# Kernel optimization log

Hardware: AMD Instinct MI355X
Metric: run time of the kernel (lower is better)

The kernel has to match this reference:

```python
import jax, jax.numpy as jnp
import numpy as np

B, T, D, H = 4, 1024, 1024, 16
HD = D // H
DFF = 2048          # ExpertTier hidden width
K = 3               # ConvTier causal kernel size
NEG = -1e9


def layernorm(x, w, b, eps=1e-5):
    m = jnp.mean(x, axis=-1, keepdims=True)
    v = jnp.var(x, axis=-1, keepdims=True)
    return (x - m) * jax.lax.rsqrt(v + eps) * w + b


def rope_cos_sin(t, hd):
    inv = 1.0 / (10000.0 ** (jnp.arange(0, hd, 2, dtype=jnp.float32) / hd))
    freqs = jnp.outer(jnp.arange(t, dtype=jnp.float32), inv)  # (T, hd/2)
    return jnp.cos(freqs), jnp.sin(freqs)


def apply_rope(x, cos, sin):
    # x: (B, H, T, hd); cos/sin: (T, hd/2)
    x1, x2 = jnp.split(x, 2, axis=-1)
    return jnp.concatenate([x1 * cos - x2 * sin, x1 * sin + x2 * cos], axis=-1)


def causal_attn(q, k, v):
    # q,k,v: (..., T, d); full causal softmax attention
    t = q.shape[-2]
    scale = 1.0 / jnp.sqrt(jnp.asarray(q.shape[-1], q.dtype))
    scores = jnp.einsum('...qd,...kd->...qk', q, k) * scale
    mask = jnp.triu(jnp.ones((t, t), dtype=bool), k=1)
    scores = jnp.where(mask, NEG, scores)
    w = jax.nn.softmax(scores, axis=-1)
    return jnp.einsum('...qk,...kd->...qd', w, v)


def setup_inputs() -> dict:
    key = jax.random.key(0)
    ks = jax.random.split(key, 16)
    ws = 0.02
    g = lambda k, shape, s: jax.random.normal(k, shape, dtype=jnp.float32) * s
    return {
        'x': g(ks[0], (B, T, D), 1.0),
        'ln1_w': jnp.ones((D,), jnp.float32), 'ln1_b': jnp.zeros((D,), jnp.float32),
        'qkv_w': g(ks[1], (D, 3 * D), ws),
        'out_w': g(ks[2], (D, D), ws),
        'ln2_w': jnp.ones((D,), jnp.float32), 'ln2_b': jnp.zeros((D,), jnp.float32),
        'router_w': g(ks[3], (D, 4), ws),
        'conv_w': g(ks[4], (D, 1, K), 0.1),             # depthwise OIW, groups=D
        'expert_w1': g(ks[5], (D, DFF), ws),
        'expert_w2': g(ks[6], (DFF, D), ws),
        'at_wq': g(ks[7], (D, D), ws),
        'at_wk': g(ks[8], (D, D), ws),
        'at_wv': g(ks[9], (D, D), ws),
        'at_wo': g(ks[10], (D, D), ws),
        'tier_gate': jnp.full((D,), 0.1, jnp.float32),
        'sink_kv_scale': jnp.asarray(0.1, jnp.float32),
    }


def reference(x, ln1_w, ln1_b, qkv_w, out_w, ln2_w, ln2_b, router_w, conv_w,
              expert_w1, expert_w2, at_wq, at_wk, at_wv, at_wo,
              tier_gate, sink_kv_scale):
    b, t, d = x.shape
    # --- backbone causal self-attention with RoPE (pre-norm) ---
    h1 = layernorm(x, ln1_w, ln1_b)
    qkv = (h1 @ qkv_w).reshape(b, t, 3, H, HD)
    q = qkv[:, :, 0].transpose(0, 2, 1, 3)  # (B,H,T,hd)
    k = qkv[:, :, 1].transpose(0, 2, 1, 3)
    v = qkv[:, :, 2].transpose(0, 2, 1, 3)
    cos, sin = rope_cos_sin(t, HD)
    q = apply_rope(q, cos, sin)
    k = apply_rope(k, cos, sin)
    ao = causal_attn(q, k, v)                         # (B,H,T,hd)
    ao = ao.transpose(0, 2, 1, 3).reshape(b, t, d) @ out_w
    x = x + ao
    # --- router + tiers ---
    h = layernorm(x, ln2_w, ln2_b)
    routing_w = jax.nn.softmax(h @ router_w, axis=-1)  # (B,T,4): conv/expert/attn/sink
    # ConvTier: depthwise causal conv (k=3) + GELU
    hc = jnp.pad(h.transpose(0, 2, 1), ((0, 0), (0, 0), (K - 1, 0)))  # (B,D,T+K-1)
    conv = jax.lax.conv_general_dilated(hc, conv_w, (1,), 'VALID',
                                        feature_group_count=d,
                                        dimension_numbers=('NCH', 'OIH', 'NCH'))
    conv_out = jax.nn.gelu(conv.transpose(0, 2, 1))   # (B,T,D)
    # ExpertTier: 2-layer GELU MLP
    expert_out = jax.nn.gelu(h @ expert_w1) @ expert_w2
    # AttentionTier: single-head causal attention
    attn2 = causal_attn(h @ at_wq, h @ at_wk, h @ at_wv) @ at_wo
    # SinkTier outputs zeros -> contributes nothing to the weighted sum
    combined = (conv_out * routing_w[..., 0:1]
                + expert_out * routing_w[..., 1:2]
                + attn2 * routing_w[..., 2:3])
    x = x + combined * tier_gate
    # sink kv scaling
    kv_scale = 1.0 - routing_w[..., 3] * (1.0 - jnp.abs(sink_kv_scale))
    x = x * kv_scale[..., None]
    return (x, routing_w)
```

## Files before the change

### kernel.cpp

```cpp
#include <hip/hip_runtime.h>

#define Bz 4
#define Tz 1024
#define Dz 1024
#define Hz 16
#define NTz (Bz*Tz)

typedef short s8v __attribute__((ext_vector_type(8)));
typedef float f4v __attribute__((ext_vector_type(4)));

__device__ __forceinline__ float bf2f(unsigned short u){
  unsigned int x = ((unsigned int)u) << 16;
  return __builtin_bit_cast(float, x);
}
__device__ __forceinline__ unsigned short f2bf(float f){
  unsigned int x = __builtin_bit_cast(unsigned int, f);
  x += 0x7fffu + ((x >> 16) & 1u);
  return (unsigned short)(x >> 16);
}
__device__ __forceinline__ float gelu_f(float x){
  float z = 1.5957691216057308f * (x + 0.044715f * x * x * x);
  return x / (1.0f + __expf(-z));
}
__device__ __forceinline__ void gl16(const unsigned short* g, unsigned short* l){
  __builtin_amdgcn_global_load_lds(
      (const __attribute__((address_space(1))) unsigned int*)g,
      (__attribute__((address_space(3))) unsigned int*)l, 16, 0, 0);
}

struct WSeg { const float* in; unsigned short* out; int R, C, blk0, bx; };
struct WPack { WSeg s[8]; };
__global__ __launch_bounds__(256) void k_convtrans_all(WPack p)
{
  __shared__ float tile[32][33];
  int bid = blockIdx.x;
  const float* in = p.s[0].in; unsigned short* out = p.s[0].out;
  int R = p.s[0].R, C = p.s[0].C, blk0 = 0, bx = p.s[0].bx;
  #pragma unroll
  for (int i = 1; i < 8; ++i) {
    if (bid >= p.s[i].blk0) {
      in = p.s[i].in; out = p.s[i].out; R = p.s[i].R; C = p.s[i].C;
      blk0 = p.s[i].blk0; bx = p.s[i].bx;
    }
  }
  int rel = bid - blk0;
  int c0 = (rel % bx) * 32, r0 = (rel / bx) * 32;
  int tx = threadIdx.x & 31, ty = threadIdx.x >> 5;
  #pragma unroll
  for (int i = 0; i < 32; i += 8)
    tile[ty + i][tx] = in[(long)(r0 + ty + i) * C + c0 + tx];
  __syncthreads();
  #pragma unroll
  for (int i = 0; i < 32; i += 8)
    out[(long)(c0 + ty + i) * R + r0 + tx] = f2bf(tile[tx][ty + i]);
}

__global__ __launch_bounds__(256) void k_convtrans_b(const unsigned short* __restrict__ in,
    unsigned short* __restrict__ out, int ld, long sIn, long sOut)
{
  __shared__ unsigned short tile[32][34];
  in  += (long)blockIdx.z * sIn;
  out += (long)blockIdx.z * sOut;
  int c0 = blockIdx.x * 32, r0 = blockIdx.y * 32;
  int tx = threadIdx.x & 31, ty = threadIdx.x >> 5;
  #pragma unroll
  for (int i = 0; i < 32; i += 8)
    tile[ty + i][tx] = in[(long)(r0 + ty + i) * ld + c0 + tx];
  __syncthreads();
  #pragma unroll
  for (int i = 0; i < 32; i += 8)
    out[(long)(c0 + ty + i) * 1024 + r0 + tx] = tile[tx][ty + i];
}

__global__ __launch_bounds__(256) void k_layernorm(const float* __restrict__ x,
    const float* __restrict__ w, const float* __restrict__ b,
    unsigned short* __restrict__ out)
{
  int row = blockIdx.x, tid = threadIdx.x;
  const float4* xp = (const float4*)(x + (long)row * Dz);
  float4 v = xp[tid];
  float s  = v.x + v.y + v.z + v.w;
  float ss = v.x*v.x + v.y*v.y + v.z*v.z + v.w*v.w;
  int lane = tid & 63, wv = tid >> 6;
  #pragma unroll
  for (int off = 32; off; off >>= 1){ s += __shfl_xor(s, off); ss += __shfl_xor(ss, off); }
  __shared__ float red[8];
  if (lane == 0){ red[wv] = s; red[4 + wv] = ss; }
  __syncthreads();
  s  = red[0] + red[1] + red[2] + red[3];
  ss = red[4] + red[5] + red[6] + red[7];
  float mean = s * (1.0f / Dz);
  float var  = ss * (1.0f / Dz) - mean * mean;
  float rstd = rsqrtf(var + 1e-5f);
  float4 wg = ((const float4*)w)[tid];
  float4 bg = ((const float4*)b)[tid];
  ushort4 ov;
  ov.x = f2bf((v.x - mean) * rstd * wg.x + bg.x);
  ov.y = f2bf((v.y - mean) * rstd * wg.y + bg.y);
  ov.z = f2bf((v.z - mean) * rstd * wg.z + bg.z);
  ov.w = f2bf((v.w - mean) * rstd * wg.w + bg.w);
  *((ushort4*)(out + (long)row * Dz) + tid) = ov;
}

__global__ __launch_bounds__(256) void k_ln_router(const float* __restrict__ x,
    const float* __restrict__ w, const float* __restrict__ b,
    const float* __restrict__ rw, unsigned short* __restrict__ out,
    float* __restrict__ rout)
{
  int row = blockIdx.x, tid = threadIdx.x;
  const float4* xp = (const float4*)(x + (long)row * Dz);
  float4 v = xp[tid];
  float s  = v.x + v.y + v.z + v.w;
  float ss = v.x*v.x + v.y*v.y + v.z*v.z + v.w*v.w;
  int lane = tid & 63, wv = tid >> 6;
  #pragma unroll
  for (int off = 32; off; off >>= 1){ s += __shfl_xor(s, off); ss += __shfl_xor(ss, off); }
  __shared__ float red[8];
  if (lane == 0){ red[wv] = s; red[4 + wv] = ss; }
  __syncthreads();
  s  = red[0] + red[1] + red[2] + red[3];
  ss = red[4] + red[5] + red[6] + red[7];
  float mean = s * (1.0f / Dz);
  float var  = ss * (1.0f / Dz) - mean * mean;
  float rstd = rsqrtf(var + 1e-5f);
  float4 wg = ((const float4*)w)[tid];
  float4 bg = ((const float4*)b)[tid];
  float h0 = (v.x - mean) * rstd * wg.x + bg.x;
  float h1 = (v.y - mean) * rstd * wg.y + bg.y;
  float h2 = (v.z - mean) * rstd * wg.z + bg.z;
  float h3 = (v.w - mean) * rstd * wg.w + bg.w;
  ushort4 ov;
  ov.x = f2bf(h0); ov.y = f2bf(h1); ov.z = f2bf(h2); ov.w = f2bf(h3);
  *((ushort4*)(out + (long)row * Dz) + tid) = ov;
  int d0 = tid * 4;
  float4 r0 = *(const float4*)(rw + (long)d0 * 4);
  float4 r1 = *(const float4*)(rw + (long)(d0 + 1) * 4);
  float4 r2 = *(const float4*)(rw + (long)(d0 + 2) * 4);
  float4 r3 = *(const float4*)(rw + (long)(d0 + 3) * 4);
  float a0 = h0*r0.x + h1*r1.x + h2*r2.x + h3*r3.x;
  float a1 = h0*r0.y + h1*r1.y + h2*r2.y + h3*r3.y;
  float a2 = h0*r0.z + h1*r1.z + h2*r2.z + h3*r3.z;
  float a3 = h0*r0.w + h1*r1.w + h2*r2.w + h3*r3.w;
  #pragma unroll
  for (int off = 32; off; off >>= 1) {
    a0 += __shfl_xor(a0, off); a1 += __shfl_xor(a1, off);
    a2 += __shfl_xor(a2, off); a3 += __shfl_xor(a3, off);
  }
  __shared__ float red2[4][4];
  if (lane == 0){ red2[wv][0] = a0; red2[wv][1] = a1; red2[wv][2] = a2; red2[wv][3] = a3; }
  __syncthreads();
  if (tid == 0) {
    float s0 = red2[0][0] + red2[1][0] + red2[2][0] + red2[3][0];
    float s1 = red2[0][1] + red2[1][1] + red2[2][1] + red2[3][1];
    float s2 = red2[0][2] + red2[1][2] + red2[2][2] + red2[3][2];
    float s3 = red2[0][3] + red2[1][3] + red2[2][3] + red2[3][3];
    float mx = fmaxf(fmaxf(s0, s1), fmaxf(s2, s3));
    float e0 = __expf(s0 - mx), e1 = __expf(s1 - mx);
    float e2 = __expf(s2 - mx), e3 = __expf(s3 - mx);
    float inv = 1.0f / (e0 + e1 + e2 + e3);
    float4 r = {e0 * inv, e1 * inv, e2 * inv, e3 * inv};
    *(float4*)(rout + (long)row * 4) = r;
  }
}

template<int MODE, int BN, bool TRIMAP, bool TRIK, bool DBUF>
__global__ __launch_bounds__(256) void k_gemm(
    const unsigned short* __restrict__ A,
    const unsigned short* __restrict__ Bt,
    float* __restrict__ Cf, unsigned short* __restrict__ Cb,
    const float* __restrict__ addsrc,
    unsigned short* __restrict__ P1, unsigned short* __restrict__ P2,
    int N, int K, int lda, int ldb,
    long sA, long sB, long sC)
{
  constexpr int BM = 128;
  constexpr int MREP = (BN == 128) ? 4 : 2;
  constexpr int NB = DBUF ? 2 : 1;
  __shared__ unsigned short As[NB][BM * 64];
  __shared__ unsigned short Bs[NB][BN * 64];
  int bm, bn;
  if (TRIMAP) {
    int li = blockIdx.x;
    int nwg = gridDim.x;
    if ((nwg & 7) == 0) li = (li & 7) * (nwg >> 3) + (li >> 3);
    int r = (int)((sqrtf(4.f * li + 1.f) - 1.f) * 0.5f);
    if ((r + 1) * (r + 2) <= li) ++r;
    if (r * (r + 1) > li) --r;
    bm = r * 128; bn = (li - r * (r + 1)) * BN;
  } else {
    int lin = blockIdx.y * gridDim.x + blockIdx.x;
    int nwg = gridDim.x * gridDim.y;
    if ((nwg & 7) == 0) lin = (lin & 7) * (nwg >> 3) + (lin >> 3);
    int cols = gridDim.x, rows = gridDim.y;
    constexpr int GM = 8;
    int in_grp = GM * cols;
    int gid = lin / in_grp;
    int fm = gid * GM;
    int gsz = min(rows - fm, GM);
    int rem = lin - gid * in_grp;
    int pm = fm + (rem % gsz);
    int pn = rem / gsz;
    if (TRIK) pm = rows - 1 - pm;
    bm = pm * BM; bn = pn * BN;
  }
  A  += (long)blockIdx.z * sA;
  Bt += (long)blockIdx.z * sB;
  int tid = threadIdx.x, w = tid >> 6, lane = tid & 63;
  int wr, wc;
  if (BN == 128) { wr = (w >> 1) * 64; wc = (w & 1) * 64; }
  else           { wr = w * 32;        wc = 0; }
  f4v acc[MREP][4];
  #pragma unroll
  for (int m = 0; m < MREP; ++m)
    #pragma unroll
    for (int n = 0; n < 4; ++n)
      acc[m][n] = (f4v){0.f, 0.f, 0.f, 0.f};

  int Keff = K;
  if (TRIK) Keff = min(K, bm + BM);

  int lrow = lane >> 3;
  int lcol = (((lane & 7) ^ lrow) * 8);
  const unsigned short* AgJ[4];
  int AsOff[4];
  #pragma unroll
  for (int j = 0; j < 4; ++j) {
    AgJ[j] = A + (long)(bm + w * 32 + j * 8 + lrow) * lda + lcol;
    AsOff[j] = (w * 32 + j * 8) * 64;
  }
  constexpr int BCH = BN / 8 / 4;
  const unsigned short* BgJ[BCH];
  int BsOff[BCH];
  #pragma unroll
  for (int j = 0; j < BCH; ++j) {
    BgJ[j] = Bt + (long)(bn + w * (BCH * 8) + j * 8 + lrow) * ldb + lcol;
    BsOff[j] = (w * (BCH * 8) + j * 8) * 64;
  }

  int fr = lane & 15, fg = lane >> 4;
  int sw = (fr & 7) * 8;

  auto stage = [&](int buf, int k0){
    #pragma unroll
    for (int j = 0; j < 4; ++j) gl16(AgJ[j] + k0, &As[buf][AsOff[j]]);
    #pragma unroll
    for (int j = 0; j < BCH; ++j) gl16(BgJ[j] + k0, &Bs[buf][BsOff[j]]);
  };
  auto compute = [&](int buf){
    #pragma unroll
    for (int kk = 0; kk < 2; ++kk) {
      int kg = (kk * 32 + fg * 8) ^ sw;
      s8v af[MREP], bfv[4];
      #pragma unroll
      for (int m = 0; m < MREP; ++m) af[m]  = *(const s8v*)&As[buf][(wr + m * 16 + fr) * 64 + kg];
      #pragma unroll
      for (int n = 0; n < 4; ++n)    bfv[n] = *(const s8v*)&Bs[buf][(wc + n * 16 + fr) * 64 + kg];
      #pragma unroll
      for (int m = 0; m < MREP; ++m)
        #pragma unroll
        for (int n = 0; n < 4; ++n)
          acc[m][n] = __builtin_amdgcn_mfma_f32_16x16x32_bf16(af[m], bfv[n], acc[m][n], 0, 0, 0);
    }
  };

  if (DBUF) {
    int cur = 0;
    stage(0, 0);
    __syncthreads();
    for (int k0 = 0; k0 < Keff; k0 += 64) {
      if (k0 + 64 < Keff) stage(cur ^ 1, k0 + 64);
      compute(cur);
      __syncthreads();
      cur ^= 1;
    }
  } else {
    for (int k0 = 0; k0 < Keff; k0 += 64) {
      __syncthreads();
      stage(0, k0);
      __syncthreads();
      compute(0);
    }
  }

  int cr0 = bm + wr + fg * 4;
  int cc0 = bn + wc + fr;

  if (MODE == 4) {
    int sect = bn >> 10;
    if (sect == 2) {
      #pragma unroll
      for (int m = 0; m < MREP; ++m)
        #pragma unroll
        for (int n = 0; n < 4; ++n)
          #pragma unroll
          for (int i = 0; i < 4; ++i) {
            int row = cr0 + m * 16 + i;
            int vcol = (bn - 2048) + wc + n * 16 + fr;
            P2[(long)row * 1024 + vcol] = f2bf(acc[m][n][i]);
          }
    } else {
      unsigned short* dst = (sect == 0) ? Cb : P1;
      float scl = (sect == 0) ? 0.125f : 1.0f;
      int head = ((bn & 1023) + wc) >> 6;
      float inv0 = exp2f(-(float)fr * 0.4152410118609203f);
      float inv1 = exp2f(-(float)(fr + 16) * 0.4152410118609203f);
      #pragma unroll
      for (int m = 0; m < MREP; ++m)
        #pragma unroll
        for (int i = 0; i < 4; ++i) {
          int row = cr0 + m * 16 + i;
          int t = row & 1023, bq = row >> 10;
          float a0 = (float)t * inv0, a1 = (float)t * inv1;
          float cs0 = __cosf(a0), sn0 = __sinf(a0);
          float cs1 = __cosf(a1), sn1 = __sinf(a1);
          float v0 = acc[m][0][i], v1 = acc[m][1][i];
          float v2 = acc[m][2][i], v3 = acc[m][3][i];
          long base = ((long)(bq * 16 + head)) * 65536 + (long)t * 64 + fr;
          dst[base]      = f2bf((v0 * cs0 - v2 * sn0) * scl);
          dst[base + 32] = f2bf((v0 * sn0 + v2 * cs0) * scl);
          dst[base + 16] = f2bf((v1 * cs1 - v3 * sn1) * scl);
          dst[base + 48] = f2bf((v1 * sn1 + v3 * cs1) * scl);
        }
    }
    return;
  }

  #pragma unroll
  for (int m = 0; m < MREP; ++m)
    #pragma unroll
    for (int n = 0; n < 4; ++n)
      #pragma unroll
      for (int i = 0; i < 4; ++i) {
        long row = cr0 + m * 16 + i, col = cc0 + n * 16;
        long idx = (long)blockIdx.z * sC + row * (long)N + col;
        float v = acc[m][n][i];
        if (MODE == 1) v += addsrc[idx];
        if (MODE == 5) { if (col < 2048) v = gelu_f(v); }
        if (MODE == 6) v *= 0.03125f;
        if (MODE <= 1) Cf[idx] = v; else Cb[idx] = f2bf(v);
      }
}

__global__ __launch_bounds__(256) void k_attn_mfma(
    const unsigned short* __restrict__ Qb, const unsigned short* __restrict__ Kb,
    const unsigned short* __restrict__ Vt, unsigned short* __restrict__ ao)
{
  __shared__ unsigned short Ks[64][72];
  __shared__ unsigned short Vs[64][72];
  __shared__ unsigned short Ps[4][16][72];
  int qb = 15 - (blockIdx.x >> 6);
  int bh = blockIdx.x & 63;
  int b = bh >> 4, h = bh & 15;
  int t0 = qb * 64;
  int tid = threadIdx.x, w = tid >> 6, lane = tid & 63;
  int fr = lane & 15, fg = lane >> 4;

  const unsigned short* qp = Qb + (long)bh * Tz * 64 + (long)(t0 + w * 16 + fr) * 64 + fg * 8;
  s8v qf[2] = { *(const s8v*)qp, *(const s8v*)(qp + 32) };

  f4v o_acc[4];
  #pragma unroll
  for (int n = 0; n < 4; ++n) o_acc[n] = (f4v){0.f, 0.f, 0.f, 0.f};
  float m_[4] = {-1e30f, -1e30f, -1e30f, -1e30f};
  float l_[4] = {0.f, 0.f, 0.f, 0.f};

  int sr = tid >> 3, sc = (tid & 7) * 8;
  const unsigned short* Kg = Kb + (long)bh * Tz * 64 + (long)sr * 64 + sc;
  const unsigned short* Vg = Vt + (long)bh * 64 * Tz + (long)sr * Tz + sc;

  uint4 pk0, pk1, pv0, pv1;
  auto loadregs = [&](int k0){
    pk0 = *(const uint4*)(Kg + (long)k0 * 64);
    pk1 = *(const uint4*)(Kg + (long)(k0 + 32) * 64);
    pv0 = *(const uint4*)(Vg + k0);
    pv1 = *(const uint4*)(Vg + (long)32 * Tz + k0);
  };
  auto storelds = [&](){
    *(uint4*)&Ks[sr][sc]      = pk0;
    *(uint4*)&Ks[sr + 32][sc] = pk1;
    *(uint4*)&Vs[sr][sc]      = pv0;
    *(uint4*)&Vs[sr + 32][sc] = pv1;
  };

  loadregs(0);
  storelds();
  __syncthreads();

  for (int kt = 0; kt <= qb; ++kt) {
    int k0 = kt * 64;
    if (kt < qb) loadregs(k0 + 64);

    f4v sacc[4];
    #pragma unroll
    for (int n = 0; n < 4; ++n) sacc[n] = (f4v){0.f, 0.f, 0.f, 0.f};
    #pragma unroll
    for (int kk = 0; kk < 2; ++kk) {
      int kg = kk * 32 + fg * 8;
      #pragma unroll
      for (int n = 0; n < 4; ++n) {
        s8v bf = *(const s8v*)&Ks[n * 16 + fr][kg];
        sacc[n] = __builtin_amdgcn_mfma_f32_16x16x32_bf16(qf[kk], bf, sacc[n], 0, 0, 0);
      }
    }

    bool full = (kt < qb);
    float p[4][4], alpha[4];
    #pragma unroll
    for (int i = 0; i < 4; ++i) {
      int trow = t0 + w * 16 + fg * 4 + i;
      float mx = -1e30f;
      #pragma unroll
      for (int n = 0; n < 4; ++n) {
        float sval = sacc[n][i];
        if (!full) {
          int key = k0 + n * 16 + fr;
          sval = (key <= trow) ? sval : -1e30f;
        }
        p[n][i] = sval;
        mx = fmaxf(mx, sval);
      }
      mx = fmaxf(mx, __shfl_xor(mx, 1));
      mx = fmaxf(mx, __shfl_xor(mx, 2));
      mx = fmaxf(mx, __shfl_xor(mx, 4));
      mx = fmaxf(mx, __shfl_xor(mx, 8));
      float mnew = fmaxf(m_[i], mx);
      alpha[i] = __expf(m_[i] - mnew);
      m_[i] = mnew;
      float ps = 0.f;
      #pragma unroll
      for (int n = 0; n < 4; ++n) {
        float pv = __expf(p[n][i] - mnew);
        p[n][i] = pv;
        ps += pv;
      }
      ps += __shfl_xor(ps, 1); ps += __shfl_xor(ps, 2);
      ps += __shfl_xor(ps, 4); ps += __shfl_xor(ps, 8);
      l_[i] = l_[i] * alpha[i] + ps;
    }
    #pragma unroll
    for (int n = 0; n < 4; ++n)
      #pragma unroll
      for (int i = 0; i < 4; ++i)
        o_acc[n][i] *= alpha[i];
    #pragma unroll
    for (int n = 0; n < 4; ++n)
      #pragma unroll
      for (int i = 0; i < 4; ++i)
        Ps[w][fg * 4 + i][n * 16 + fr] = f2bf(p[n][i]);

    #pragma unroll
    for (int kk = 0; kk < 2; ++kk) {
      int kg = kk * 32 + fg * 8;
      s8v pa = *(const s8v*)&Ps[w][fr][kg];
      #pragma unroll
      for (int n = 0; n < 4; ++n) {
        s8v vb = *(const s8v*)&Vs[n * 16 + fr][kg];
        o_acc[n] = __builtin_amdgcn_mfma_f32_16x16x32_bf16(pa, vb, o_acc[n], 0, 0, 0);
      }
    }

    if (kt < qb) {
      __syncthreads();
      storelds();
      __syncthreads();
    }
  }

  float inv[4];
  #pragma unroll
  for (int i = 0; i < 4; ++i) inv[i] = 1.0f / l_[i];
  #pragma unroll
  for (int n = 0; n < 4; ++n)
    #pragma unroll
    for (int i = 0; i < 4; ++i) {
      int t = t0 + w * 16 + fg * 4 + i;
      ao[((long)(b * Tz + t)) * Dz + h * 64 + n * 16 + fr] = f2bf(o_acc[n][i] * inv[i]);
    }
}

__global__ __launch_bounds__(256) void k_softmax_causal(const unsigned short* __restrict__ S,
    unsigned short* __restrict__ P)
{
  long row = blockIdx.x;
  int t = (int)(row & (Tz - 1));
  int tid = threadIdx.x;
  const unsigned short* sp = S + row * Tz;
  ushort4 v = ((const ushort4*)sp)[tid];
  float vv[4];
  vv[0] = (tid*4 + 0 <= t) ? bf2f(v.x) : -1e30f;
  vv[1] = (tid*4 + 1 <= t) ? bf2f(v.y) : -1e30f;
  vv[2] = (tid*4 + 2 <= t) ? bf2f(v.z) : -1e30f;
  vv[3] = (tid*4 + 3 <= t) ? bf2f(v.w) : -1e30f;
  float mx = fmaxf(fmaxf(vv[0], vv[1]), fmaxf(vv[2], vv[3]));
  int lane = tid & 63, wv = tid >> 6;
  #pragma unroll
  for (int off = 32; off; off >>= 1) mx = fmaxf(mx, __shfl_xor(mx, off));
  __shared__ float red[8];
  if (lane == 0) red[wv] = mx;
  __syncthreads();
  mx = fmaxf(fmaxf(red[0], red[1]), fmaxf(red[2], red[3]));
  float p[4];
  float s = 0.f;
  #pragma unroll
  for (int i = 0; i < 4; ++i){ p[i] = __expf(vv[i] - mx); s += p[i]; }
  #pragma unroll
  for (int off = 32; off; off >>= 1) s += __shfl_xor(s, off);
  if (lane == 0) red[4 + wv] = s;
  __syncthreads();
  s = red[4] + red[5] + red[6] + red[7];
  float inv = 1.0f / s;
  ushort4 ov;
  ov.x = f2bf(p[0] * inv); ov.y = f2bf(p[1] * inv);
  ov.z = f2bf(p[2] * inv); ov.w = f2bf(p[3] * inv);
  *((ushort4*)(P + row * Tz) + tid) = ov;
}

__global__ __launch_bounds__(256) void k_combine(
    const float* __restrict__ x2, const unsigned short* __restrict__ hbf,
    const unsigned short* __restrict__ eoa, const unsigned short* __restrict__ eob,
    const unsigned short* __restrict__ ap,
    const float* __restrict__ rout, const float* __restrict__ convw,
    const float* __restrict__ tg, const float* __restrict__ sinkp,
    float* __restrict__ outx)
{
  int row = blockIdx.x, tid = threadIdx.x;
  int t = row & (Tz - 1), b = row >> 10;
  int d0 = tid * 4;
  float4 x4 = *(const float4*)(x2 + (long)row * Dz + d0);
  ushort4 ea = *(const ushort4*)(eoa + (long)row * Dz + d0);
  ushort4 eb = *(const ushort4*)(eob + (long)row * Dz + d0);
  ushort4 a4 = *(const ushort4*)(ap + (long)row * Dz + d0);
  float4 t4 = *(const float4*)(tg + d0);
  float4 r4 = *(const float4*)(rout + (long)row * 4);
  float sks = fabsf(sinkp[0]);
  float kv = 1.0f - r4.w * (1.0f - sks);
  const float4* cwp = (const float4*)(convw + (long)d0 * 3);
  float4 c0 = cwp[0], c1 = cwp[1], c2 = cwp[2];
  float cwf[12] = {c0.x, c0.y, c0.z, c0.w, c1.x, c1.y, c1.z, c1.w, c2.x, c2.y, c2.z, c2.w};
  float hv[3][4];
  #pragma unroll
  for (int tap = 0; tap < 3; ++tap) {
    int tt = t - 2 + tap;
    if (tt >= 0) {
      ushort4 hu = *((const ushort4*)(hbf + ((long)(b * Tz + tt)) * Dz + d0));
      hv[tap][0] = bf2f(hu.x); hv[tap][1] = bf2f(hu.y);
      hv[tap][2] = bf2f(hu.z); hv[tap][3] = bf2f(hu.w);
    } else {
      hv[tap][0] = 0.f; hv[tap][1] = 0.f; hv[tap][2] = 0.f; hv[tap][3] = 0.f;
    }
  }
  float ov[4];
  float xi[4] = {x4.x, x4.y, x4.z, x4.w};
  float ei[4] = {bf2f(ea.x) + bf2f(eb.x), bf2f(ea.y) + bf2f(eb.y),
                 bf2f(ea.z) + bf2f(eb.z), bf2f(ea.w) + bf2f(eb.w)};
  float ai[4] = {bf2f(a4.x), bf2f(a4.y), bf2f(a4.z), bf2f(a4.w)};
  float ti[4] = {t4.x, t4.y, t4.z, t4.w};
  #pragma unroll
  for (int i = 0; i < 4; ++i) {
    float conv = hv[0][i] * cwf[i*3 + 0] + hv[1][i] * cwf[i*3 + 1] + hv[2][i] * cwf[i*3 + 2];
    float comb = gelu_f(conv) * r4.x + ei[i] * r4.y + ai[i] * r4.z;
    ov[i] = (xi[i] + comb * ti[i]) * kv;
  }
  float4 res = {ov[0], ov[1], ov[2], ov[3]};
  *(float4*)(outx + (long)row * Dz + d0) = res;
}

extern "C" void kernel_launch(void* const* d_in, const int* in_sizes, int n_in,
                              void* d_out, int out_size, void* d_ws, size_t ws_size,
                              hipStream_t stream) {
  (void)in_sizes; (void)n_in; (void)out_size; (void)ws_size;
  const float* x       = (const float*)d_in[0];
  const float* ln1_w   = (const float*)d_in[1];
  const float* ln1_b   = (const float*)d_in[2];
  const float* qkv_w   = (const float*)d_in[3];
  const float* out_w   = (const float*)d_in[4];
  const float* ln2_w   = (const float*)d_in[5];
  const float* ln2_b   = (const float*)d_in[6];
  const float* router_w= (const float*)d_in[7];
  const float* conv_w  = (const float*)d_in[8];
  const float* ew1     = (const float*)d_in[9];
  const float* ew2     = (const float*)d_in[10];
  const float* at_wq   = (const float*)d_in[11];
  const float* at_wk   = (const float*)d_in[12];
  const float* at_wv   = (const float*)d_in[13];
  const float* at_wo   = (const float*)d_in[14];
  const float* tg      = (const float*)d_in[15];
  const float* sinkp   = (const float*)d_in[16];
  float* outx = (float*)d_out;
  float* rout = outx + (size_t)NTz * Dz;

  char* ws = (char*)d_ws;
  size_t off = 0;
  auto alloc = [&](size_t bytes) -> char* {
    char* p = ws + off;
    off += (bytes + 255) & ~(size_t)255;
    return p;
  };
  const long TD = (long)Tz * Dz, TT = (long)Tz * Tz;

  unsigned short* w_qkvt  = (unsigned short*)alloc((size_t)3072*1024*2);
  unsigned short* w_outt  = (unsigned short*)alloc((size_t)1024*1024*2);
  unsigned short* w_tiert = (unsigned short*)alloc((size_t)5120*1024*2);
  unsigned short* w_ew2t  = (unsigned short*)alloc((size_t)1024*2048*2);
  unsigned short* w_wot   = (unsigned short*)alloc((size_t)1024*1024*2);
  unsigned short* h1bf    = (unsigned short*)alloc((size_t)NTz*Dz*2);
  unsigned short* tierb   = (unsigned short*)alloc((size_t)NTz*5120*2);
  unsigned short* aobf    = (unsigned short*)alloc((size_t)NTz*Dz*2);
  float*          x2f     = (float*)alloc((size_t)NTz*Dz*4);
  unsigned short* hbf     = (unsigned short*)alloc((size_t)NTz*Dz*2);
  unsigned short* Pbf     = (unsigned short*)alloc((size_t)Bz*Tz*Tz*2);
  unsigned short* v2tbf   = (unsigned short*)alloc((size_t)NTz*Dz*2);
  unsigned short* a2obf   = (unsigned short*)alloc((size_t)NTz*Dz*2);
  unsigned short* eofb    = (unsigned short*)alloc((size_t)NTz*Dz*2);
  unsigned short* a2pb    = (unsigned short*)alloc((size_t)NTz*Dz*2);
  unsigned short* Sbf     = (unsigned short*)alloc((size_t)Bz*Tz*Tz*2);

  unsigned short* Qb = (unsigned short*)x2f;
  unsigned short* Kb = Pbf;
  unsigned short* Vb = tierb;
  unsigned short* Vt = a2pb;
  unsigned short* eofb2 = h1bf;
  long eoDelta = (long)(eofb2 - eofb);

  dim3 blk(256);

  WPack wp;
  wp.s[0] = {qkv_w, w_qkvt,                         1024, 3072, 0,     96};
  wp.s[1] = {out_w, w_outt,                         1024, 1024, 3072,  32};
  wp.s[2] = {ew1,   w_tiert,                        1024, 2048, 4096,  64};
  wp.s[3] = {at_wq, w_tiert + 2048*1024,            1024, 1024, 6144,  32};
  wp.s[4] = {at_wk, w_tiert + 3072*1024,            1024, 1024, 7168,  32};
  wp.s[5] = {at_wv, w_tiert + (size_t)4096*1024,    1024, 1024, 8192,  32};
  wp.s[6] = {ew2,   w_ew2t,                         2048, 1024, 9216,  32};
  wp.s[7] = {at_wo, w_wot,                          1024, 1024, 11264, 32};
  k_convtrans_all<<<dim3(12288), blk, 0, stream>>>(wp);

  k_layernorm<<<NTz, blk, 0, stream>>>(x, ln1_w, ln1_b, h1bf);
  k_gemm<4,128,false,false,true><<<dim3(24, 32), blk, 0, stream>>>(h1bf, w_qkvt,
      nullptr, Qb, nullptr, Kb, Vb, 3072, 1024, 1024, 1024, 0, 0, 0);
  k_convtrans_b<<<dim3(32, 32, 4), blk, 0, stream>>>(Vb, Vt, 1024, TD, TD);
  k_attn_mfma<<<dim3(1024), blk, 0, stream>>>(Qb, Kb, Vt, aobf);
  k_gemm<1,64,false,false,true><<<dim3(16, 32), blk, 0, stream>>>(aobf, w_outt, x2f,
      nullptr, x, nullptr, nullptr, 1024, 1024, 1024, 1024, 0, 0, 0);
  k_ln_router<<<NTz, blk, 0, stream>>>(x2f, ln2_w, ln2_b, router_w, hbf, rout);
  k_gemm<5,128,false,false,true><<<dim3(40, 32), blk, 0, stream>>>(hbf, w_tiert,
      nullptr, tierb, nullptr, nullptr, nullptr, 5120, 1024, 1024, 1024, 0, 0, 0);
  k_gemm<3,64,false,false,true><<<dim3(16, 32, 2), blk, 0, stream>>>(tierb, w_ew2t,
      nullptr, eofb, nullptr, nullptr, nullptr, 1024, 1024, 5120, 2048,
      1024, 1024, eoDelta);
  k_convtrans_b<<<dim3(32, 32, 4), blk, 0, stream>>>(tierb + 4096, v2tbf, 5120,
      (long)Tz*5120, TD);
  k_gemm<6,64,true,false,true><<<dim3(72, 1, 4), blk, 0, stream>>>(tierb + 2048,
      tierb + 3072, nullptr, Sbf, nullptr, nullptr, nullptr,
      1024, 1024, 5120, 5120, (long)Tz*5120, (long)Tz*5120, TT);
  k_softmax_causal<<<NTz, blk, 0, stream>>>(Sbf, Pbf);
  k_gemm<3,64,false,true,true><<<dim3(16, 8, 4), blk, 0, stream>>>(Pbf, v2tbf, nullptr,
      a2obf, nullptr, nullptr, nullptr, 1024, 1024, 1024, 1024, TT, TD, TD);
  k_gemm<3,64,false,false,true><<<dim3(16, 32), blk, 0, stream>>>(a2obf, w_wot, nullptr,
      a2pb, nullptr, nullptr, nullptr, 1024, 1024, 1024, 1024, 0, 0, 0);
  k_combine<<<NTz, blk, 0, stream>>>(x2f, hbf, eofb, eofb2, a2pb, rout, conv_w,
      tg, sinkp, outx);
}
```

Baseline: 302.1 us.

## Add 256x256 8-wave pipelined GEMM for fused tier projection

Replaces the 128x128-tile tier projection GEMM (h @ [expert_w1|wq|wk|wv]) with a dedicated 512-thread kernel using 256x256 output tiles split into four quadrant phases. It uses an 8-slot LDS ring fed by direct global-to-LDS loads, with explicit vmcnt waits and barriers, so loads for the next K step overlap MFMA work on the current one. It also adds XCD-aware block remapping with grouped tile ordering for L2 reuse, plus s_setprio around the MFMA bursts. This trades higher LDS and register use per block, and hardcoded shapes, for more data reuse per tile and latency hiding.

```diff
diff --git a/kernel.cpp b/kernel.cpp
--- a/kernel.cpp
+++ b/kernel.cpp
@@ -27,6 +27,9 @@
       (const __attribute__((address_space(1))) unsigned int*)g,
       (__attribute__((address_space(3))) unsigned int*)l, 16, 0, 0);
 }
+
+#define VM(n) asm volatile("s_waitcnt vmcnt(" #n ")" ::: "memory")
+#define BAR() asm volatile("s_barrier" ::: "memory")
 
 struct WSeg { const float* in; unsigned short* out; int R, C, blk0, bx; };
 struct WPack { WSeg s[8]; };
@@ -161,6 +164,137 @@
     float4 r = {e0 * inv, e1 * inv, e2 * inv, e3 * inv};
     *(float4*)(rout + (long)row * 4) = r;
   }
+}
+
+#define PHASE(MQ, NQ, SA, SB) do { \
+  s8v af0[4], af1[4], bg0[2], bg1[2]; \
+  _Pragma("unroll") \
+  for (int m = 0; m < 4; ++m) { \
+    int rr = (wmr + m * 16 + fr) * 64; \
+    af0[m] = *(const s8v*)&HT[SA][rr + ((fg * 8) ^ sw)]; \
+    af1[m] = *(const s8v*)&HT[SA][rr + ((32 + fg * 8) ^ sw)]; \
+  } \
+  _Pragma("unroll") \
+  for (int n = 0; n < 2; ++n) { \
+    int rr = (wnr + n * 16 + fr) * 64; \
+    bg0[n] = *(const s8v*)&HT[SB][rr + ((fg * 8) ^ sw)]; \
+    bg1[n] = *(const s8v*)&HT[SB][rr + ((32 + fg * 8) ^ sw)]; \
+  } \
+  __builtin_amdgcn_s_setprio(1); \
+  _Pragma("unroll") \
+  for (int m = 0; m < 4; ++m) \
+    _Pragma("unroll") \
+    for (int n = 0; n < 2; ++n) { \
+      acc[MQ][NQ][m][n] = __builtin_amdgcn_mfma_f32_16x16x32_bf16(af0[m], bg0[n], acc[MQ][NQ][m][n], 0, 0, 0); \
+      acc[MQ][NQ][m][n] = __builtin_amdgcn_mfma_f32_16x16x32_bf16(af1[m], bg1[n], acc[MQ][NQ][m][n], 0, 0, 0); \
+    } \
+  __builtin_amdgcn_s_setprio(0); \
+} while (0)
+
+#define STAGE(SLOT, S0, S1, KT) do { \
+  gl16(S0 + (long)(KT) * 64, &HT[SLOT][dst0]); \
+  gl16(S1 + (long)(KT) * 64, &HT[SLOT][dst1]); \
+} while (0)
+
+__global__ __launch_bounds__(512, 2) void k_gemm8(
+    const unsigned short* __restrict__ A,
+    const unsigned short* __restrict__ Bt,
+    unsigned short* __restrict__ Cb)
+{
+  __shared__ unsigned short HT[8][128 * 64];
+  int lin = blockIdx.y * gridDim.x + blockIdx.x;
+  int nwg = gridDim.x * gridDim.y;
+  if ((nwg & 7) == 0) lin = (lin & 7) * (nwg >> 3) + (lin >> 3);
+  int cols = gridDim.x, rows = gridDim.y;
+  int in_grp = 8 * cols;
+  int gid = lin / in_grp;
+  int fm = gid * 8;
+  int gsz = min(rows - fm, 8);
+  int rem = lin - gid * in_grp;
+  int pm = fm + (rem % gsz);
+  int pn = rem / gsz;
+  int bm = pm * 256, bn = pn * 256;
+
+  int tid = threadIdx.x, w = tid >> 6, lane = tid & 63;
+  int fr = lane & 15, fg = lane >> 4;
+  int sw = (fr & 7) * 8;
+  int wmr = (w >> 2) * 64;
+  int wnr = (w & 3) * 32;
+  int lrow8 = lane >> 3;
+  int lcol = ((lane & 7) ^ lrow8) * 8;
+  int dst0 = (w * 8) * 64, dst1 = (64 + w * 8) * 64;
+
+  const unsigned short* sA00 = A  + (long)(bm +   0 + w * 8 + lrow8) * 1024 + lcol;
+  const unsigned short* sA01 = sA00 + (long)64  * 1024;
+  const unsigned short* sA10 = sA00 + (long)128 * 1024;
+  const unsigned short* sA11 = sA00 + (long)192 * 1024;
+  const unsigned short* sB00 = Bt + (long)(bn +   0 + w * 8 + lrow8) * 1024 + lcol;
+  const unsigned short* sB01 = sB00 + (long)64  * 1024;
+  const unsigned short* sB10 = sB00 + (long)128 * 1024;
+  const unsigned short* sB11 = sB00 + (long)192 * 1024;
+
+  f4v acc[2][2][4][2];
+  #pragma unroll
+  for (int a = 0; a < 2; ++a)
+    #pragma unroll
+    for (int b = 0; b < 2; ++b)
+      #pragma unroll
+      for (int m = 0; m < 4; ++m)
+        #pragma unroll
+        for (int n = 0; n < 2; ++n)
+          acc[a][b][m][n] = (f4v){0.f, 0.f, 0.f, 0.f};
+
+  STAGE(0, sA00, sA01, 0);
+  STAGE(1, sB00, sB01, 0);
+  STAGE(2, sB10, sB11, 0);
+  STAGE(3, sA10, sA11, 0);
+  STAGE(4, sA00, sA01, 1);
+  VM(2); BAR();
+
+  for (int k = 0; k < 15; ++k) {
+    int g  = (k & 1) << 2;
+    int g1 = g ^ 4;
+    STAGE(g1 + 1, sB00, sB01, k + 1);
+    VM(8); BAR();
+    PHASE(0, 0, g + 0, g + 1);
+    BAR();
+    STAGE(g1 + 2, sB10, sB11, k + 1);
+    VM(8); BAR();
+    PHASE(0, 1, g + 0, g + 2);
+    BAR();
+    STAGE(g1 + 3, sA10, sA11, k + 1);
+    VM(8); BAR();
+    PHASE(1, 1, g + 3, g + 2);
+    BAR();
+    if (k < 14) STAGE(g + 0, sA00, sA01, k + 2);
+    VM(8); BAR();
+    PHASE(1, 0, g + 3, g + 1);
+    BAR();
+  }
+  {
+    VM(4); BAR(); PHASE(0, 0, 4, 5); BAR();
+    VM(2); BAR(); PHASE(0, 1, 4, 6); BAR();
+    VM(0); BAR(); PHASE(1, 1, 7, 6); BAR();
+    BAR();        PHASE(1, 0, 7, 5);
+  }
+
+  int cr = bm + wmr + fg * 4, cc = bn + wnr + fr;
+  #pragma unroll
+  for (int Mq = 0; Mq < 2; ++Mq)
+    #pragma unroll
+    for (int Nq = 0; Nq < 2; ++Nq)
+      #pragma unroll
+      for (int m = 0; m < 4; ++m)
+        #pragma unroll
+        for (int n = 0; n < 2; ++n)
+          #pragma unroll
+          for (int i = 0; i < 4; ++i) {
+            long row = cr + Mq * 128 + m * 16 + i;
+            long col = cc + Nq * 128 + n * 16;
+            float v = acc[Mq][Nq][m][n][i];
+            if (col < 2048) v = gelu_f(v);
+            Cb[row * 5120 + col] = f2bf(v);
+          }
 }
 
 template<int MODE, int BN, bool TRIMAP, bool TRIK, bool DBUF>
@@ -335,7 +469,6 @@
         long idx = (long)blockIdx.z * sC + row * (long)N + col;
         float v = acc[m][n][i];
         if (MODE == 1) v += addsrc[idx];
-        if (MODE == 5) { if (col < 2048) v = gelu_f(v); }
         if (MODE == 6) v *= 0.03125f;
         if (MODE <= 1) Cf[idx] = v; else Cb[idx] = f2bf(v);
       }
@@ -643,8 +776,7 @@
   k_gemm<1,64,false,false,true><<<dim3(16, 32), blk, 0, stream>>>(aobf, w_outt, x2f,
       nullptr, x, nullptr, nullptr, 1024, 1024, 1024, 1024, 0, 0, 0);
   k_ln_router<<<NTz, blk, 0, stream>>>(x2f, ln2_w, ln2_b, router_w, hbf, rout);
-  k_gemm<5,128,false,false,true><<<dim3(40, 32), blk, 0, stream>>>(hbf, w_tiert,
-      nullptr, tierb, nullptr, nullptr, nullptr, 5120, 1024, 1024, 1024, 0, 0, 0);
+  k_gemm8<<<dim3(20, 16), dim3(512), 0, stream>>>(hbf, w_tiert, tierb);
   k_gemm<3,64,false,false,true><<<dim3(16, 32, 2), blk, 0, stream>>>(tierb, w_ew2t,
       nullptr, eofb, nullptr, nullptr, nullptr, 1024, 1024, 5120, 2048,
       1024, 1024, eoDelta);
```

New measurement: 313.2 us. 3.7% more time.
